# Kernel tuning notes

Hardware: AMD Instinct MI355X
Metric: run time of the kernel (lower is better)

Reference implementation:

```python
import jax, jax.numpy as jnp
import numpy as np

NUM_NODES = 113      # nodes (ROIs) per graph, from __init__ default
NUM_GRAPHS = 4096    # graphs in the batch
IN_DIM, HID, EMB = 3, 128, 1024
GROUPS = 8
EPS = 1e-5


def _kaiming(key, fan_in, fan_out_dim, shape):
    # kaiming_normal_(mode='fan_out', nonlinearity='leaky_relu') with default a=sqrt(5)->gain irrelevant here;
    # torch uses gain = sqrt(2/(1+0.01^2)) for leaky_relu default slope; simple faithful-scale normal init.
    gain = jnp.sqrt(2.0 / (1.0 + 0.01 ** 2)).astype(jnp.float32)
    std = gain / jnp.sqrt(jnp.float32(fan_out_dim))
    return jax.random.normal(key, shape, dtype=jnp.float32) * std


def setup_inputs() -> dict:
    key = jax.random.key(0)
    ks = jax.random.split(key, 8)
    N = NUM_GRAPHS * NUM_NODES
    x = jax.random.normal(ks[0], (N, IN_DIM), dtype=jnp.float32)
    batch = jnp.repeat(jnp.arange(NUM_GRAPHS, dtype=jnp.int32), NUM_NODES)
    return {
        "x": x,
        "roi_scaler": jnp.ones((NUM_NODES, IN_DIM), dtype=jnp.float32),
        "W1": _kaiming(ks[1], IN_DIM, HID, (IN_DIM, HID)),
        "b1": jnp.zeros((HID,), jnp.float32),
        "gn_g": jnp.ones((HID,), jnp.float32),
        "gn_b": jnp.zeros((HID,), jnp.float32),
        "W2": _kaiming(ks[2], HID, HID, (HID, HID)),
        "b2": jnp.zeros((HID,), jnp.float32),
        "W3": _kaiming(ks[3], HID, 512, (HID, 512)),
        "b3": jnp.zeros((512,), jnp.float32),
        "bn_g": jnp.ones((512,), jnp.float32),
        "bn_b": jnp.zeros((512,), jnp.float32),
        "W4": _kaiming(ks[4], 512, EMB, (512, EMB)),
        "b4": jnp.zeros((EMB,), jnp.float32),
        "batch": batch,
    }


def _group_norm(h, gamma, beta):
    # torch GroupNorm on [N, C]: per-row, per-group normalization
    N, C = h.shape
    hg = h.reshape(N, GROUPS, C // GROUPS)
    mu = hg.mean(axis=-1, keepdims=True)
    var = hg.var(axis=-1, keepdims=True)
    hn = ((hg - mu) * jax.lax.rsqrt(var + EPS)).reshape(N, C)
    return hn * gamma + beta


def reference(x, roi_scaler, W1, b1, gn_g, gn_b, W2, b2, W3, b3, bn_g, bn_b, W4, b4, batch):
    # per-ROI learned scaling, tiled across graphs (node order is graph-major)
    h = x * jnp.tile(roi_scaler, (NUM_GRAPHS, 1))            # [N, 3]
    # node_net: Linear -> GroupNorm(8) -> LeakyReLU(0.2) -> Linear
    h = h @ W1 + b1                                          # [N, 128]
    h = _group_norm(h, gn_g, gn_b)
    h = jnp.where(h > 0, h, 0.2 * h)
    h = h @ W2 + b2                                          # [N, 128]
    # global_max_pool: segment max over graph id
    z = jax.ops.segment_max(h, batch, num_segments=NUM_GRAPHS)  # [G, 128]
    # projection: Linear -> BatchNorm1d (batch stats, no running stats) -> ReLU -> Linear
    p = z @ W3 + b3                                          # [G, 512]
    mu = p.mean(axis=0)
    var = p.var(axis=0)
    p = (p - mu) * jax.lax.rsqrt(var + EPS) * bn_g + bn_b
    p = jax.nn.relu(p)
    out = p @ W4 + b4                                        # [G, 1024]
    # F.normalize(p=2, dim=1)
    nrm = jnp.sqrt(jnp.sum(out * out, axis=1, keepdims=True))
    return out / jnp.maximum(nrm, 1e-12)
```

## Files before the change

### kernel.cpp

```cpp
#include <hip/hip_runtime.h>
#include <hip/hip_bf16.h>

typedef _Float16 f16_8 __attribute__((ext_vector_type(8)));
typedef _Float16 f16_2 __attribute__((ext_vector_type(2)));
typedef float f32x4 __attribute__((ext_vector_type(4)));

#define NNODES 113
#define NGRAPH 4096

#define Z_OFF    0u
#define PSUM_OFF 0u
#define PSQ_OFF  65536u
#define PSN_OFF  131072u
#define P_OFF    2097152u
#define GC_OFF   10485760u
#define SA_OFF   10489856u
#define SD_OFF   10491904u
#define W2P_OFF  10493952u
#define W4P_OFF  10559488u

__global__ __launch_bounds__(256) void k0_prep(
    const float* __restrict__ W2, const float* __restrict__ W4,
    const float* __restrict__ W1, const float* __restrict__ b1,
    _Float16* __restrict__ w2p, _Float16* __restrict__ w4p,
    float* __restrict__ gc) {
  int b = blockIdx.x, t = threadIdx.x;
  if (b < 256) {
    __shared__ _Float16 T[32 * 72];
    int kt = b >> 4, nc = b & 15;
    int row = t >> 3, c8 = (t & 7) * 8;
    const float* src = &W4[(kt * 32 + row) * 1024 + nc * 64 + c8];
    float4 a0 = *(const float4*)src;
    float4 a1 = *(const float4*)(src + 4);
    f16_8 v = {(_Float16)a0.x, (_Float16)a0.y, (_Float16)a0.z, (_Float16)a0.w,
               (_Float16)a1.x, (_Float16)a1.y, (_Float16)a1.z, (_Float16)a1.w};
    *(f16_8*)&T[row * 72 + c8] = v;
    __syncthreads();
    int ntl = t >> 6, L = t & 63;
    f16_8 w;
#pragma unroll
    for (int j = 0; j < 8; j++)
      w[j] = T[((L >> 4) * 8 + j) * 72 + ntl * 16 + (L & 15)];
    *(f16_8*)&w4p[((kt * 64 + nc * 4 + ntl) * 64 + L) * 8] = w;
  } else if (b < 264) {
    int q0 = (b - 256) * 256 + t;
    int L = q0 & 63, nt = (q0 >> 6) & 7, kt = q0 >> 9;
    f16_8 v;
#pragma unroll
    for (int j = 0; j < 8; j++)
      v[j] = (_Float16)W2[(kt * 32 + ((L >> 4) << 3) + j) * 128 + (nt << 4) + (L & 15)];
    *(f16_8*)&w2p[((kt * 8 + nt) * 64 + L) * 8] = v;
  } else {
    if (t < 128) {
      float a0 = W1[t], a1 = W1[128 + t], a2 = W1[256 + t], bb = b1[t];
      float p[14] = {a0, a1, a2, bb,
                     a0 * a0, 2.f * a0 * a1, 2.f * a0 * a2,
                     a1 * a1, 2.f * a1 * a2, a2 * a2,
                     2.f * bb * a0, 2.f * bb * a1, 2.f * bb * a2, bb * bb};
#pragma unroll
      for (int m = 1; m < 16; m <<= 1)
#pragma unroll
        for (int k = 0; k < 14; k++) p[k] += __shfl_xor(p[k], m, 64);
      if ((t & 15) == 0) {
        int gg = t >> 4;
#pragma unroll
        for (int k = 0; k < 4; k++) gc[gg * 16 + k] = p[k] * 0.0625f;
#pragma unroll
        for (int k = 4; k < 14; k++) gc[gg * 16 + k] = p[k];
      }
    }
  }
}

__global__ __launch_bounds__(256, 4) void k1_nodenet(
    const float* __restrict__ x, const float* __restrict__ roi,
    const float* __restrict__ W1, const float* __restrict__ b1,
    const float* __restrict__ gn_g, const float* __restrict__ gn_b,
    const _Float16* __restrict__ w2p, const float* __restrict__ b2,
    const float* __restrict__ gc, float* __restrict__ z) {
  __shared__ float4 xs4[NNODES];
  __shared__ f16_2 st[904];
  __shared__ _Float16 A[128 * 136];
  int t = threadIdx.x, g = blockIdx.x;
  int lane = t & 63, wv = t >> 6, quad = lane >> 4, l16 = lane & 15;

  int gs = t & 7;
  float gcv[14];
#pragma unroll
  for (int j = 0; j < 14; j++) gcv[j] = gc[gs * 16 + j];

  int o = t & 15;
  float pw0[8], pw1[8], pw2[8], pb[8], pg[8], pbe[8];
#pragma unroll
  for (int j = 0; j < 8; j++) {
    int c = o * 8 + j;
    pw0[j] = W1[c]; pw1[j] = W1[128 + c]; pw2[j] = W1[256 + c];
    pb[j] = b1[c];  pg[j] = gn_g[c];      pbe[j] = gn_b[c];
  }

  f16_8 bh[4][2];
#pragma unroll
  for (int kt = 0; kt < 4; kt++)
#pragma unroll
    for (int ni = 0; ni < 2; ni++)
      bh[kt][ni] = *(const f16_8*)&w2p[((kt * 8 + wv * 2 + ni) * 64 + lane) * 8];

  for (int i = t; i < NNODES * 3; i += 256) {
    float v = x[g * (NNODES * 3) + i] * roi[i];
    ((float*)xs4)[(i / 3) * 4 + (i % 3)] = v;
  }
  __syncthreads();

  for (int it = t; it < 904; it += 256) {
    int n = it >> 3;
    float4 xv = xs4[n];
    float mu = fmaf(xv.z, gcv[2], fmaf(xv.y, gcv[1], fmaf(xv.x, gcv[0], gcv[3])));
    float qf = fmaf(xv.z, gcv[12], fmaf(xv.y, gcv[11], fmaf(xv.x, gcv[10], gcv[13])));
    float u0 = fmaf(xv.z, gcv[6], fmaf(xv.y, gcv[5], xv.x * gcv[4]));
    qf = fmaf(xv.x, u0, qf);
    float u1 = fmaf(xv.z, gcv[8], xv.y * gcv[7]);
    qf = fmaf(xv.y, u1, qf);
    qf = fmaf(xv.z * xv.z, gcv[9], qf);
    float var = fmaxf(qf * 0.0625f - mu * mu, 0.0f);
    float inv = rsqrtf(var + 1e-5f);
    f16_2 s2 = {(_Float16)inv, (_Float16)(-mu * inv)};
    st[it] = s2;
  }
  __syncthreads();

  for (int it = t; it < 2048; it += 256) {
    int n = it >> 4;
    f16_8 hv;
    if (n < NNODES) {
      float4 xv = xs4[n];
      f16_2 s2 = st[n * 8 + (o >> 1)];
      float ia = (float)s2[0], ib = (float)s2[1];
#pragma unroll
      for (int j = 0; j < 8; j++) {
        float h = fmaf(xv.z, pw2[j], fmaf(xv.y, pw1[j], fmaf(xv.x, pw0[j], pb[j])));
        float y = fmaf(fmaf(h, ia, ib), pg[j], pbe[j]);
        y = (y > 0.0f) ? y : 0.2f * y;
        hv[j] = (_Float16)y;
      }
    } else {
#pragma unroll
      for (int j = 0; j < 8; j++) hv[j] = (_Float16)0.f;
    }
    *(f16_8*)&A[n * 136 + o * 8] = hv;
  }
  __syncthreads();

  f32x4 acc[2][8];
#pragma unroll
  for (int a = 0; a < 2; a++)
#pragma unroll
    for (int m = 0; m < 8; m++) acc[a][m] = (f32x4){0.f, 0.f, 0.f, 0.f};

#pragma unroll
  for (int kt = 0; kt < 4; kt++) {
    f16_8 ah[8];
#pragma unroll
    for (int mt = 0; mt < 8; mt++)
      ah[mt] = *(const f16_8*)&A[(mt * 16 + l16) * 136 + kt * 32 + quad * 8];
#pragma unroll
    for (int ni = 0; ni < 2; ni++)
#pragma unroll
      for (int mt = 0; mt < 8; mt++)
        acc[ni][mt] = __builtin_amdgcn_mfma_f32_16x16x32_f16(ah[mt], bh[kt][ni], acc[ni][mt], 0, 0, 0);
  }

#pragma unroll
  for (int ni = 0; ni < 2; ni++) {
    int nt = wv * 2 + ni;
    float m = -3.4e38f;
#pragma unroll
    for (int mt = 0; mt < 8; mt++)
#pragma unroll
      for (int r = 0; r < 4; r++) {
        int row = mt * 16 + quad * 4 + r;
        if (row < NNODES) m = fmaxf(m, acc[ni][mt][r]);
      }
    m = fmaxf(m, __shfl_xor(m, 16, 64));
    m = fmaxf(m, __shfl_xor(m, 32, 64));
    if (quad == 0) {
      int col = nt * 16 + l16;
      z[g * 128 + col] = m + b2[col];
    }
  }
}

__global__ __launch_bounds__(256) void k2_proj(
    const float* __restrict__ z, const float* __restrict__ W3,
    const float* __restrict__ b3, float* __restrict__ p) {
  __shared__ float zs[16 * 128];
  int t = threadIdx.x;
  int rb = blockIdx.x >> 2, cbb = blockIdx.x & 3;
  int gr0 = rb * 16, cc0 = cbb * 128;
  for (int i = t; i < 2048; i += 256) zs[i] = z[gr0 * 128 + i];
  int cg = t & 31, rg = t >> 5;
  int cc = cc0 + cg * 4;
  float4 bb = *(const float4*)&b3[cc];
  float acc0[4] = {0.f, 0.f, 0.f, 0.f}, acc1[4] = {0.f, 0.f, 0.f, 0.f};
  __syncthreads();

#pragma unroll 8
  for (int k = 0; k < 128; k++) {
    float4 w = *(const float4*)&W3[k * 512 + cc];
    float z0 = zs[rg * 256 + k];
    float z1 = zs[rg * 256 + 128 + k];
    acc0[0] = fmaf(z0, w.x, acc0[0]); acc0[1] = fmaf(z0, w.y, acc0[1]);
    acc0[2] = fmaf(z0, w.z, acc0[2]); acc0[3] = fmaf(z0, w.w, acc0[3]);
    acc1[0] = fmaf(z1, w.x, acc1[0]); acc1[1] = fmaf(z1, w.y, acc1[1]);
    acc1[2] = fmaf(z1, w.z, acc1[2]); acc1[3] = fmaf(z1, w.w, acc1[3]);
  }
  int r0 = gr0 + rg * 2;
  float4 o0 = make_float4(acc0[0] + bb.x, acc0[1] + bb.y, acc0[2] + bb.z, acc0[3] + bb.w);
  float4 o1 = make_float4(acc1[0] + bb.x, acc1[1] + bb.y, acc1[2] + bb.z, acc1[3] + bb.w);
  *(float4*)&p[r0 * 512 + cc] = o0;
  *(float4*)&p[(r0 + 1) * 512 + cc] = o1;
}

__global__ __launch_bounds__(256) void k2b_partial(
    const float* __restrict__ p, float* __restrict__ psum, float* __restrict__ psq) {
  int t = threadIdx.x, b = blockIdx.x;
  int r0 = b * 128;
  float s0 = 0.f, q0 = 0.f, s1 = 0.f, q1 = 0.f;
  for (int r = 0; r < 128; r++) {
    float v0 = p[(r0 + r) * 512 + t];
    float v1 = p[(r0 + r) * 512 + t + 256];
    s0 += v0; q0 = fmaf(v0, v0, q0);
    s1 += v1; q1 = fmaf(v1, v1, q1);
  }
  psum[b * 512 + t] = s0;
  psum[b * 512 + t + 256] = s1;
  psq[b * 512 + t] = q0;
  psq[b * 512 + t + 256] = q1;
}

__global__ __launch_bounds__(512) void k3_stats(
    const float* __restrict__ psum, const float* __restrict__ psq,
    const float* __restrict__ bn_g, const float* __restrict__ bn_b,
    float* __restrict__ sa, float* __restrict__ sd) {
  int c = threadIdx.x;
  float s = 0.f, q = 0.f;
#pragma unroll 4
  for (int b = 0; b < 32; b++) {
    s += psum[b * 512 + c];
    q += psq[b * 512 + c];
  }
  float mu = s * (1.0f / 4096.0f);
  float var = fmaxf(q * (1.0f / 4096.0f) - mu * mu, 0.0f);
  float sc = bn_g[c] * rsqrtf(var + 1e-5f);
  sa[c] = sc;
  sd[c] = bn_b[c] - mu * sc;
}

__global__ __launch_bounds__(256) void k4a_gemm(
    const float* __restrict__ p, const float* __restrict__ sa,
    const float* __restrict__ sd, const _Float16* __restrict__ w4p,
    const float* __restrict__ b4, float* __restrict__ out,
    float* __restrict__ psn) {
  __shared__ _Float16 T[2][64 * 40];
  __shared__ float sas[512], sds[512];
  __shared__ float rred[4 * 64];
  int t = threadIdx.x;
  int rb = blockIdx.x & 63, cb = blockIdx.x >> 6;
  int lane = t & 63, wv = t >> 6, quad = lane >> 4, l16 = lane & 15;

  for (int i = t; i < 512; i += 256) { sas[i] = sa[i]; sds[i] = sd[i]; }

  int srow = t >> 2, sc8 = (t & 3) * 8;
  const float* prow = &p[(rb * 64 + srow) * 512];
  float4 pa0 = *(const float4*)&prow[sc8];
  float4 pa1 = *(const float4*)&prow[sc8 + 4];
  f16_8 bfr[2];
#pragma unroll
  for (int ni = 0; ni < 2; ni++)
    bfr[ni] = *(const f16_8*)&w4p[((cb * 8 + wv * 2 + ni) * 64 + lane) * 8];
  __syncthreads();

  {
    f16_8 v;
#pragma unroll
    for (int j = 0; j < 4; j++)
      v[j] = (_Float16)fmaxf(fmaf(((float*)&pa0)[j], sas[sc8 + j], sds[sc8 + j]), 0.0f);
#pragma unroll
    for (int j = 0; j < 4; j++)
      v[4 + j] = (_Float16)fmaxf(fmaf(((float*)&pa1)[j], sas[sc8 + 4 + j], sds[sc8 + 4 + j]), 0.0f);
    *(f16_8*)&T[0][srow * 40 + sc8] = v;
  }
  __syncthreads();

  f32x4 acc[2][4];
#pragma unroll
  for (int a = 0; a < 2; a++)
#pragma unroll
    for (int m = 0; m < 4; m++) acc[a][m] = (f32x4){0.f, 0.f, 0.f, 0.f};

  for (int kt = 0; kt < 16; kt++) {
    int nb = kt + 1;
    float4 na0, na1;
    if (nb < 16) {
      na0 = *(const float4*)&prow[nb * 32 + sc8];
      na1 = *(const float4*)&prow[nb * 32 + sc8 + 4];
    }
    f16_8 bc0 = bfr[0], bc1 = bfr[1];
    if (nb < 16) {
#pragma unroll
      for (int ni = 0; ni < 2; ni++)
        bfr[ni] = *(const f16_8*)&w4p[((nb * 64 + cb * 8 + wv * 2 + ni) * 64 + lane) * 8];
    }
    const _Float16* Tb = &T[kt & 1][0];
#pragma unroll
    for (int mt = 0; mt < 4; mt++) {
      f16_8 af = *(const f16_8*)&Tb[(mt * 16 + l16) * 40 + quad * 8];
      acc[0][mt] = __builtin_amdgcn_mfma_f32_16x16x32_f16(af, bc0, acc[0][mt], 0, 0, 0);
      acc[1][mt] = __builtin_amdgcn_mfma_f32_16x16x32_f16(af, bc1, acc[1][mt], 0, 0, 0);
    }
    if (nb < 16) {
      int kc = nb * 32 + sc8;
      f16_8 v;
#pragma unroll
      for (int j = 0; j < 4; j++)
        v[j] = (_Float16)fmaxf(fmaf(((float*)&na0)[j], sas[kc + j], sds[kc + j]), 0.0f);
#pragma unroll
      for (int j = 0; j < 4; j++)
        v[4 + j] = (_Float16)fmaxf(fmaf(((float*)&na1)[j], sas[kc + 4 + j], sds[kc + 4 + j]), 0.0f);
      *(f16_8*)&T[nb & 1][srow * 40 + sc8] = v;
    }
    __syncthreads();
  }

  float rsq[4][4];
#pragma unroll
  for (int mt = 0; mt < 4; mt++)
#pragma unroll
    for (int r = 0; r < 4; r++) rsq[mt][r] = 0.0f;
#pragma unroll
  for (int ni = 0; ni < 2; ni++) {
    int col = cb * 128 + (wv * 2 + ni) * 16 + l16;
    float bv = b4[col];
#pragma unroll
    for (int mt = 0; mt < 4; mt++)
#pragma unroll
      for (int r = 0; r < 4; r++) {
        float v = acc[ni][mt][r] + bv;
        out[(rb * 64 + mt * 16 + quad * 4 + r) * 1024 + col] = v;
        rsq[mt][r] = fmaf(v, v, rsq[mt][r]);
      }
  }
#pragma unroll
  for (int m = 1; m < 16; m <<= 1)
#pragma unroll
    for (int mt = 0; mt < 4; mt++)
#pragma unroll
      for (int r = 0; r < 4; r++) rsq[mt][r] += __shfl_xor(rsq[mt][r], m, 64);
  if (l16 == 0) {
#pragma unroll
    for (int mt = 0; mt < 4; mt++)
#pragma unroll
      for (int r = 0; r < 4; r++)
        rred[wv * 64 + mt * 16 + quad * 4 + r] = rsq[mt][r];
  }
  __syncthreads();
  if (t < 64) {
    float s = rred[t] + rred[64 + t] + rred[128 + t] + rred[192 + t];
    psn[cb * 4096 + rb * 64 + t] = s;
  }
}

__global__ __launch_bounds__(256) void k4b_norm(
    float* __restrict__ out, const float* __restrict__ psn) {
  int t = threadIdx.x;
  int row = blockIdx.x * 4 + (t >> 6);
  float s = 0.f;
#pragma unroll
  for (int cb = 0; cb < 8; cb++) s += psn[cb * 4096 + row];
  float inv = 1.0f / fmaxf(sqrtf(s), 1e-12f);
  int c0 = (t & 63) * 4;
#pragma unroll
  for (int it = 0; it < 4; it++) {
    float4 v = *(const float4*)&out[row * 1024 + it * 256 + c0];
    v.x *= inv; v.y *= inv; v.z *= inv; v.w *= inv;
    *(float4*)&out[row * 1024 + it * 256 + c0] = v;
  }
}

extern "C" void kernel_launch(void* const* d_in, const int* in_sizes, int n_in,
                              void* d_out, int out_size, void* d_ws, size_t ws_size,
                              hipStream_t stream) {
  const float* x   = (const float*)d_in[0];
  const float* roi = (const float*)d_in[1];
  const float* W1  = (const float*)d_in[2];
  const float* b1  = (const float*)d_in[3];
  const float* gng = (const float*)d_in[4];
  const float* gnb = (const float*)d_in[5];
  const float* W2  = (const float*)d_in[6];
  const float* b2  = (const float*)d_in[7];
  const float* W3  = (const float*)d_in[8];
  const float* b3  = (const float*)d_in[9];
  const float* bng = (const float*)d_in[10];
  const float* bnb = (const float*)d_in[11];
  const float* W4  = (const float*)d_in[12];
  const float* b4  = (const float*)d_in[13];
  float* out = (float*)d_out;

  char* ws = (char*)d_ws;
  float*    z    = (float*)(ws + Z_OFF);
  float*    psum = (float*)(ws + PSUM_OFF);
  float*    psq  = (float*)(ws + PSQ_OFF);
  float*    psn  = (float*)(ws + PSN_OFF);
  float*    p    = (float*)(ws + P_OFF);
  float*    gc   = (float*)(ws + GC_OFF);
  float*    sa   = (float*)(ws + SA_OFF);
  float*    sd   = (float*)(ws + SD_OFF);
  _Float16* w2p  = (_Float16*)(ws + W2P_OFF);
  _Float16* w4p  = (_Float16*)(ws + W4P_OFF);

  k0_prep<<<265, 256, 0, stream>>>(W2, W4, W1, b1, w2p, w4p, gc);
  k1_nodenet<<<NGRAPH, 256, 0, stream>>>(x, roi, W1, b1, gng, gnb, w2p, b2, gc, z);
  k2_proj<<<1024, 256, 0, stream>>>(z, W3, b3, p);
  k2b_partial<<<32, 256, 0, stream>>>(p, psum, psq);
  k3_stats<<<1, 512, 0, stream>>>(psum, psq, bng, bnb, sa, sd);
  k4a_gemm<<<512, 256, 0, stream>>>(p, sa, sd, w4p, b4, out, psn);
  k4b_norm<<<1024, 256, 0, stream>>>(out, psn);
}
```

Baseline: 181.3 us.

## Fuse BN stats into projection, store fp16 p, and fuse final GEMM with L2 norm

The projection kernel now writes p in fp16 and emits per-block column sum and sum-of-squares partials, which removes the separate partial-stats pass. The final GEMM is restructured so each block owns 16 full rows across all 1024 columns. That lets the row L2 normalization happen in-register and drops the k4b read-modify-write of the output. The node-net kernel also computes the GroupNorm stats inline instead of through a shared-memory table, removing a barrier. The trade-offs are a single-block stats kernel that now loops over 256 partials, only 256 blocks for the final GEMM, and each block streaming all of W4 from global memory, plus fp16 rounding of p before BatchNorm.

```diff
diff --git a/kernel.cpp b/kernel.cpp
--- a/kernel.cpp
+++ b/kernel.cpp
@@ -2,17 +2,16 @@
 #include <hip/hip_bf16.h>
 
 typedef _Float16 f16_8 __attribute__((ext_vector_type(8)));
-typedef _Float16 f16_2 __attribute__((ext_vector_type(2)));
+typedef _Float16 f16_4 __attribute__((ext_vector_type(4)));
 typedef float f32x4 __attribute__((ext_vector_type(4)));
 
 #define NNODES 113
 #define NGRAPH 4096
 
 #define Z_OFF    0u
-#define PSUM_OFF 0u
-#define PSQ_OFF  65536u
-#define PSN_OFF  131072u
-#define P_OFF    2097152u
+#define PH_OFF   2097152u
+#define PSUM_OFF 6291456u
+#define PSQ_OFF  6815744u
 #define GC_OFF   10485760u
 #define SA_OFF   10489856u
 #define SD_OFF   10491904u
@@ -79,17 +78,16 @@
     const _Float16* __restrict__ w2p, const float* __restrict__ b2,
     const float* __restrict__ gc, float* __restrict__ z) {
   __shared__ float4 xs4[NNODES];
-  __shared__ f16_2 st[904];
   __shared__ _Float16 A[128 * 136];
   int t = threadIdx.x, g = blockIdx.x;
   int lane = t & 63, wv = t >> 6, quad = lane >> 4, l16 = lane & 15;
 
-  int gs = t & 7;
+  int o = t & 15;
+  int gq = o >> 1;
   float gcv[14];
 #pragma unroll
-  for (int j = 0; j < 14; j++) gcv[j] = gc[gs * 16 + j];
-
-  int o = t & 15;
+  for (int j = 0; j < 14; j++) gcv[j] = gc[gq * 16 + j];
+
   float pw0[8], pw1[8], pw2[8], pb[8], pg[8], pbe[8];
 #pragma unroll
   for (int j = 0; j < 8; j++) {
@@ -108,23 +106,6 @@
   for (int i = t; i < NNODES * 3; i += 256) {
     float v = x[g * (NNODES * 3) + i] * roi[i];
     ((float*)xs4)[(i / 3) * 4 + (i % 3)] = v;
-  }
-  __syncthreads();
-
-  for (int it = t; it < 904; it += 256) {
-    int n = it >> 3;
-    float4 xv = xs4[n];
-    float mu = fmaf(xv.z, gcv[2], fmaf(xv.y, gcv[1], fmaf(xv.x, gcv[0], gcv[3])));
-    float qf = fmaf(xv.z, gcv[12], fmaf(xv.y, gcv[11], fmaf(xv.x, gcv[10], gcv[13])));
-    float u0 = fmaf(xv.z, gcv[6], fmaf(xv.y, gcv[5], xv.x * gcv[4]));
-    qf = fmaf(xv.x, u0, qf);
-    float u1 = fmaf(xv.z, gcv[8], xv.y * gcv[7]);
-    qf = fmaf(xv.y, u1, qf);
-    qf = fmaf(xv.z * xv.z, gcv[9], qf);
-    float var = fmaxf(qf * 0.0625f - mu * mu, 0.0f);
-    float inv = rsqrtf(var + 1e-5f);
-    f16_2 s2 = {(_Float16)inv, (_Float16)(-mu * inv)};
-    st[it] = s2;
   }
   __syncthreads();
 
@@ -133,8 +114,16 @@
     f16_8 hv;
     if (n < NNODES) {
       float4 xv = xs4[n];
-      f16_2 s2 = st[n * 8 + (o >> 1)];
-      float ia = (float)s2[0], ib = (float)s2[1];
+      float mu = fmaf(xv.z, gcv[2], fmaf(xv.y, gcv[1], fmaf(xv.x, gcv[0], gcv[3])));
+      float qf = fmaf(xv.z, gcv[12], fmaf(xv.y, gcv[11], fmaf(xv.x, gcv[10], gcv[13])));
+      float u0 = fmaf(xv.z, gcv[6], fmaf(xv.y, gcv[5], xv.x * gcv[4]));
+      qf = fmaf(xv.x, u0, qf);
+      float u1 = fmaf(xv.z, gcv[8], xv.y * gcv[7]);
+      qf = fmaf(xv.y, u1, qf);
+      qf = fmaf(xv.z * xv.z, gcv[9], qf);
+      float var = fmaxf(qf * 0.0625f - mu * mu, 0.0f);
+      float ia = rsqrtf(var + 1e-5f);
+      float ib = -mu * ia;
 #pragma unroll
       for (int j = 0; j < 8; j++) {
         float h = fmaf(xv.z, pw2[j], fmaf(xv.y, pw1[j], fmaf(xv.x, pw0[j], pb[j])));
@@ -191,8 +180,11 @@
 
 __global__ __launch_bounds__(256) void k2_proj(
     const float* __restrict__ z, const float* __restrict__ W3,
-    const float* __restrict__ b3, float* __restrict__ p) {
+    const float* __restrict__ b3, _Float16* __restrict__ ph,
+    float* __restrict__ psum, float* __restrict__ psq) {
   __shared__ float zs[16 * 128];
+  __shared__ float reds[8 * 128];
+  __shared__ float redq[8 * 128];
   int t = threadIdx.x;
   int rb = blockIdx.x >> 2, cbb = blockIdx.x & 3;
   int gr0 = rb * 16, cc0 = cbb * 128;
@@ -200,7 +192,7 @@
   int cg = t & 31, rg = t >> 5;
   int cc = cc0 + cg * 4;
   float4 bb = *(const float4*)&b3[cc];
-  float acc0[4] = {0.f, 0.f, 0.f, 0.f}, acc1[4] = {0.f, 0.f, 0.f, 0.f};
+  float a0[4] = {0.f, 0.f, 0.f, 0.f}, a1[4] = {0.f, 0.f, 0.f, 0.f};
   __syncthreads();
 
 #pragma unroll 8
@@ -208,33 +200,37 @@
     float4 w = *(const float4*)&W3[k * 512 + cc];
     float z0 = zs[rg * 256 + k];
     float z1 = zs[rg * 256 + 128 + k];
-    acc0[0] = fmaf(z0, w.x, acc0[0]); acc0[1] = fmaf(z0, w.y, acc0[1]);
-    acc0[2] = fmaf(z0, w.z, acc0[2]); acc0[3] = fmaf(z0, w.w, acc0[3]);
-    acc1[0] = fmaf(z1, w.x, acc1[0]); acc1[1] = fmaf(z1, w.y, acc1[1]);
-    acc1[2] = fmaf(z1, w.z, acc1[2]); acc1[3] = fmaf(z1, w.w, acc1[3]);
+    a0[0] = fmaf(z0, w.x, a0[0]); a0[1] = fmaf(z0, w.y, a0[1]);
+    a0[2] = fmaf(z0, w.z, a0[2]); a0[3] = fmaf(z0, w.w, a0[3]);
+    a1[0] = fmaf(z1, w.x, a1[0]); a1[1] = fmaf(z1, w.y, a1[1]);
+    a1[2] = fmaf(z1, w.z, a1[2]); a1[3] = fmaf(z1, w.w, a1[3]);
   }
   int r0 = gr0 + rg * 2;
-  float4 o0 = make_float4(acc0[0] + bb.x, acc0[1] + bb.y, acc0[2] + bb.z, acc0[3] + bb.w);
-  float4 o1 = make_float4(acc1[0] + bb.x, acc1[1] + bb.y, acc1[2] + bb.z, acc1[3] + bb.w);
-  *(float4*)&p[r0 * 512 + cc] = o0;
-  *(float4*)&p[(r0 + 1) * 512 + cc] = o1;
-}
-
-__global__ __launch_bounds__(256) void k2b_partial(
-    const float* __restrict__ p, float* __restrict__ psum, float* __restrict__ psq) {
-  int t = threadIdx.x, b = blockIdx.x;
-  int r0 = b * 128;
-  float s0 = 0.f, q0 = 0.f, s1 = 0.f, q1 = 0.f;
-  for (int r = 0; r < 128; r++) {
-    float v0 = p[(r0 + r) * 512 + t];
-    float v1 = p[(r0 + r) * 512 + t + 256];
-    s0 += v0; q0 = fmaf(v0, v0, q0);
-    s1 += v1; q1 = fmaf(v1, v1, q1);
-  }
-  psum[b * 512 + t] = s0;
-  psum[b * 512 + t + 256] = s1;
-  psq[b * 512 + t] = q0;
-  psq[b * 512 + t + 256] = q1;
+  f16_4 h0, h1;
+  float s[4], q[4];
+#pragma unroll
+  for (int j = 0; j < 4; j++) {
+    float v0 = a0[j] + ((float*)&bb)[j];
+    float v1 = a1[j] + ((float*)&bb)[j];
+    h0[j] = (_Float16)v0; h1[j] = (_Float16)v1;
+    s[j] = v0 + v1;
+    q[j] = fmaf(v0, v0, v1 * v1);
+  }
+  *(f16_4*)&ph[r0 * 512 + cc] = h0;
+  *(f16_4*)&ph[(r0 + 1) * 512 + cc] = h1;
+#pragma unroll
+  for (int j = 0; j < 4; j++) {
+    reds[rg * 128 + cg * 4 + j] = s[j];
+    redq[rg * 128 + cg * 4 + j] = q[j];
+  }
+  __syncthreads();
+  if (t < 128) {
+    float ss = 0.f, qq = 0.f;
+#pragma unroll
+    for (int r = 0; r < 8; r++) { ss += reds[r * 128 + t]; qq += redq[r * 128 + t]; }
+    psum[rb * 512 + cc0 + t] = ss;
+    psq[rb * 512 + cc0 + t] = qq;
+  }
 }
 
 __global__ __launch_bounds__(512) void k3_stats(
@@ -243,8 +239,8 @@
     float* __restrict__ sa, float* __restrict__ sd) {
   int c = threadIdx.x;
   float s = 0.f, q = 0.f;
-#pragma unroll 4
-  for (int b = 0; b < 32; b++) {
+#pragma unroll 8
+  for (int b = 0; b < 256; b++) {
     s += psum[b * 512 + c];
     q += psq[b * 512 + c];
   }
@@ -255,134 +251,86 @@
   sd[c] = bn_b[c] - mu * sc;
 }
 
-__global__ __launch_bounds__(256) void k4a_gemm(
-    const float* __restrict__ p, const float* __restrict__ sa,
+__global__ __launch_bounds__(256) void k4_final(
+    const _Float16* __restrict__ ph, const float* __restrict__ sa,
     const float* __restrict__ sd, const _Float16* __restrict__ w4p,
-    const float* __restrict__ b4, float* __restrict__ out,
-    float* __restrict__ psn) {
-  __shared__ _Float16 T[2][64 * 40];
+    const float* __restrict__ b4, float* __restrict__ out) {
+  __shared__ _Float16 T[16 * 520];
   __shared__ float sas[512], sds[512];
-  __shared__ float rred[4 * 64];
+  __shared__ float rred[64];
   int t = threadIdx.x;
-  int rb = blockIdx.x & 63, cb = blockIdx.x >> 6;
+  int gr0 = blockIdx.x * 16;
   int lane = t & 63, wv = t >> 6, quad = lane >> 4, l16 = lane & 15;
 
   for (int i = t; i < 512; i += 256) { sas[i] = sa[i]; sds[i] = sd[i]; }
-
-  int srow = t >> 2, sc8 = (t & 3) * 8;
-  const float* prow = &p[(rb * 64 + srow) * 512];
-  float4 pa0 = *(const float4*)&prow[sc8];
-  float4 pa1 = *(const float4*)&prow[sc8 + 4];
-  f16_8 bfr[2];
-#pragma unroll
-  for (int ni = 0; ni < 2; ni++)
-    bfr[ni] = *(const f16_8*)&w4p[((cb * 8 + wv * 2 + ni) * 64 + lane) * 8];
   __syncthreads();
 
   {
-    f16_8 v;
-#pragma unroll
-    for (int j = 0; j < 4; j++)
-      v[j] = (_Float16)fmaxf(fmaf(((float*)&pa0)[j], sas[sc8 + j], sds[sc8 + j]), 0.0f);
-#pragma unroll
-    for (int j = 0; j < 4; j++)
-      v[4 + j] = (_Float16)fmaxf(fmaf(((float*)&pa1)[j], sas[sc8 + 4 + j], sds[sc8 + 4 + j]), 0.0f);
-    *(f16_8*)&T[0][srow * 40 + sc8] = v;
-  }
-  __syncthreads();
-
-  f32x4 acc[2][4];
-#pragma unroll
-  for (int a = 0; a < 2; a++)
-#pragma unroll
-    for (int m = 0; m < 4; m++) acc[a][m] = (f32x4){0.f, 0.f, 0.f, 0.f};
+    int row = t >> 4, seg = t & 15;
+    const _Float16* src = &ph[(gr0 + row) * 512 + seg * 32];
+#pragma unroll
+    for (int c4 = 0; c4 < 4; c4++) {
+      f16_8 pv = *(const f16_8*)&src[c4 * 8];
+      f16_8 tv;
+#pragma unroll
+      for (int j = 0; j < 8; j++) {
+        int k = seg * 32 + c4 * 8 + j;
+        float v = fmaf((float)pv[j], sas[k], sds[k]);
+        tv[j] = (_Float16)fmaxf(v, 0.0f);
+      }
+      *(f16_8*)&T[row * 520 + seg * 32 + c4 * 8] = tv;
+    }
+  }
+  __syncthreads();
+
+  f32x4 acc[16];
+#pragma unroll
+  for (int ni = 0; ni < 16; ni++) acc[ni] = (f32x4){0.f, 0.f, 0.f, 0.f};
 
   for (int kt = 0; kt < 16; kt++) {
-    int nb = kt + 1;
-    float4 na0, na1;
-    if (nb < 16) {
-      na0 = *(const float4*)&prow[nb * 32 + sc8];
-      na1 = *(const float4*)&prow[nb * 32 + sc8 + 4];
-    }
-    f16_8 bc0 = bfr[0], bc1 = bfr[1];
-    if (nb < 16) {
-#pragma unroll
-      for (int ni = 0; ni < 2; ni++)
-        bfr[ni] = *(const f16_8*)&w4p[((nb * 64 + cb * 8 + wv * 2 + ni) * 64 + lane) * 8];
-    }
-    const _Float16* Tb = &T[kt & 1][0];
-#pragma unroll
-    for (int mt = 0; mt < 4; mt++) {
-      f16_8 af = *(const f16_8*)&Tb[(mt * 16 + l16) * 40 + quad * 8];
-      acc[0][mt] = __builtin_amdgcn_mfma_f32_16x16x32_f16(af, bc0, acc[0][mt], 0, 0, 0);
-      acc[1][mt] = __builtin_amdgcn_mfma_f32_16x16x32_f16(af, bc1, acc[1][mt], 0, 0, 0);
-    }
-    if (nb < 16) {
-      int kc = nb * 32 + sc8;
-      f16_8 v;
-#pragma unroll
-      for (int j = 0; j < 4; j++)
-        v[j] = (_Float16)fmaxf(fmaf(((float*)&na0)[j], sas[kc + j], sds[kc + j]), 0.0f);
-#pragma unroll
-      for (int j = 0; j < 4; j++)
-        v[4 + j] = (_Float16)fmaxf(fmaf(((float*)&na1)[j], sas[kc + 4 + j], sds[kc + 4 + j]), 0.0f);
-      *(f16_8*)&T[nb & 1][srow * 40 + sc8] = v;
-    }
-    __syncthreads();
-  }
-
-  float rsq[4][4];
-#pragma unroll
-  for (int mt = 0; mt < 4; mt++)
-#pragma unroll
-    for (int r = 0; r < 4; r++) rsq[mt][r] = 0.0f;
-#pragma unroll
-  for (int ni = 0; ni < 2; ni++) {
-    int col = cb * 128 + (wv * 2 + ni) * 16 + l16;
+    f16_8 af = *(const f16_8*)&T[l16 * 520 + kt * 32 + quad * 8];
+#pragma unroll
+    for (int ni = 0; ni < 16; ni++) {
+      f16_8 bf = *(const f16_8*)&w4p[((kt * 64 + wv * 16 + ni) * 64 + lane) * 8];
+      acc[ni] = __builtin_amdgcn_mfma_f32_16x16x32_f16(af, bf, acc[ni], 0, 0, 0);
+    }
+  }
+
+  float rsq[4] = {0.f, 0.f, 0.f, 0.f};
+#pragma unroll
+  for (int ni = 0; ni < 16; ni++) {
+    int col = wv * 256 + ni * 16 + l16;
     float bv = b4[col];
 #pragma unroll
-    for (int mt = 0; mt < 4; mt++)
-#pragma unroll
-      for (int r = 0; r < 4; r++) {
-        float v = acc[ni][mt][r] + bv;
-        out[(rb * 64 + mt * 16 + quad * 4 + r) * 1024 + col] = v;
-        rsq[mt][r] = fmaf(v, v, rsq[mt][r]);
-      }
+    for (int r = 0; r < 4; r++) {
+      float v = acc[ni][r] + bv;
+      acc[ni][r] = v;
+      rsq[r] = fmaf(v, v, rsq[r]);
+    }
   }
 #pragma unroll
   for (int m = 1; m < 16; m <<= 1)
 #pragma unroll
-    for (int mt = 0; mt < 4; mt++)
-#pragma unroll
-      for (int r = 0; r < 4; r++) rsq[mt][r] += __shfl_xor(rsq[mt][r], m, 64);
+    for (int r = 0; r < 4; r++) rsq[r] += __shfl_xor(rsq[r], m, 64);
   if (l16 == 0) {
 #pragma unroll
-    for (int mt = 0; mt < 4; mt++)
-#pragma unroll
-      for (int r = 0; r < 4; r++)
-        rred[wv * 64 + mt * 16 + quad * 4 + r] = rsq[mt][r];
-  }
-  __syncthreads();
-  if (t < 64) {
-    float s = rred[t] + rred[64 + t] + rred[128 + t] + rred[192 + t];
-    psn[cb * 4096 + rb * 64 + t] = s;
-  }
-}
-
-__global__ __launch_bounds__(256) void k4b_norm(
-    float* __restrict__ out, const float* __restrict__ psn) {
-  int t = threadIdx.x;
-  int row = blockIdx.x * 4 + (t >> 6);
-  float s = 0.f;
-#pragma unroll
-  for (int cb = 0; cb < 8; cb++) s += psn[cb * 4096 + row];
-  float inv = 1.0f / fmaxf(sqrtf(s), 1e-12f);
-  int c0 = (t & 63) * 4;
-#pragma unroll
-  for (int it = 0; it < 4; it++) {
-    float4 v = *(const float4*)&out[row * 1024 + it * 256 + c0];
-    v.x *= inv; v.y *= inv; v.z *= inv; v.w *= inv;
-    *(float4*)&out[row * 1024 + it * 256 + c0] = v;
+    for (int r = 0; r < 4; r++) rred[wv * 16 + quad * 4 + r] = rsq[r];
+  }
+  __syncthreads();
+
+  float inv[4];
+#pragma unroll
+  for (int r = 0; r < 4; r++) {
+    int row = quad * 4 + r;
+    float ss = rred[row] + rred[16 + row] + rred[32 + row] + rred[48 + row];
+    inv[r] = 1.0f / fmaxf(sqrtf(ss), 1e-12f);
+  }
+#pragma unroll
+  for (int ni = 0; ni < 16; ni++) {
+    int col = wv * 256 + ni * 16 + l16;
+#pragma unroll
+    for (int r = 0; r < 4; r++)
+      out[(gr0 + quad * 4 + r) * 1024 + col] = acc[ni][r] * inv[r];
   }
 }
 
@@ -407,10 +355,9 @@
 
   char* ws = (char*)d_ws;
   float*    z    = (float*)(ws + Z_OFF);
+  _Float16* ph   = (_Float16*)(ws + PH_OFF);
   float*    psum = (float*)(ws + PSUM_OFF);
   float*    psq  = (float*)(ws + PSQ_OFF);
-  float*    psn  = (float*)(ws + PSN_OFF);
-  float*    p    = (float*)(ws + P_OFF);
   float*    gc   = (float*)(ws + GC_OFF);
   float*    sa   = (float*)(ws + SA_OFF);
   float*    sd   = (float*)(ws + SD_OFF);
@@ -419,9 +366,7 @@
 
   k0_prep<<<265, 256, 0, stream>>>(W2, W4, W1, b1, w2p, w4p, gc);
   k1_nodenet<<<NGRAPH, 256, 0, stream>>>(x, roi, W1, b1, gng, gnb, w2p, b2, gc, z);
-  k2_proj<<<1024, 256, 0, stream>>>(z, W3, b3, p);
-  k2b_partial<<<32, 256, 0, stream>>>(p, psum, psq);
+  k2_proj<<<1024, 256, 0, stream>>>(z, W3, b3, ph, psum, psq);
   k3_stats<<<1, 512, 0, stream>>>(psum, psq, bng, bnb, sa, sd);
-  k4a_gemm<<<512, 256, 0, stream>>>(p, sa, sd, w4p, b4, out, psn);
-  k4b_norm<<<1024, 256, 0, stream>>>(out, psn);
-}
+  k4_final<<<256, 256, 0, stream>>>(ph, sa, sd, w4p, b4, out);
+}
```

Result: slower. 224.6 us (+23.8%).
